# Performance work log

Hardware: AMD Instinct MI355X
Metric: run time of the kernel (lower is better)

The kernel has to match this reference:

```python
import jax, jax.numpy as jnp
import numpy as np

B, T, D_MODEL = 2, 2048, 2048
N_HEAD, N_KV, HD = 32, 8, 64


def _rope_tables(T, hd, base=10000.0):
    # standard rotary tables, (T, hd) with frequencies repeated over both halves
    inv_freq = 1.0 / (base ** (np.arange(0, hd // 2, dtype=np.float32) / (hd // 2)))
    t = np.arange(T, dtype=np.float32)
    freqs = np.outer(t, inv_freq)            # (T, hd/2)
    emb = np.concatenate([freqs, freqs], axis=-1)  # (T, hd)
    return jnp.asarray(np.cos(emb)), jnp.asarray(np.sin(emb))


def setup_inputs() -> dict:
    key = jax.random.key(0)
    ks = jax.random.split(key, 5)
    cos, sin = _rope_tables(T, HD)
    s = 0.02
    return {
        "x": jax.random.normal(ks[0], (B, T, D_MODEL), jnp.float32),
        "cos": cos,
        "sin": sin,
        "Wq": jax.random.normal(ks[1], (N_HEAD * HD, D_MODEL), jnp.float32) * s,
        "Wk": jax.random.normal(ks[2], (N_KV * HD, D_MODEL), jnp.float32) * s,
        "Wv": jax.random.normal(ks[3], (N_KV * HD, D_MODEL), jnp.float32) * s,
        "Wo": jax.random.normal(ks[4], (D_MODEL, N_HEAD * HD), jnp.float32) * s,
    }


def _apply_rope(x, cos, sin):
    # x: (B, H, T, D); cos/sin: (T, D)
    D = x.shape[-1]
    x1, x2 = x[..., : D // 2], x[..., D // 2 :]
    rot = jnp.concatenate([-x2, x1], axis=-1)
    c = cos[: x.shape[-2]][None, None]
    s = sin[: x.shape[-2]][None, None]
    return x * c + rot * s


def reference(x, cos, sin, Wq, Wk, Wv, Wo):
    Bv, Tv, _ = x.shape
    q = (x @ Wq.T).reshape(Bv, Tv, N_HEAD, HD).transpose(0, 2, 1, 3)  # (B,H,T,D)
    k = (x @ Wk.T).reshape(Bv, Tv, N_KV, HD).transpose(0, 2, 1, 3)    # (B,Hkv,T,D)
    v = (x @ Wv.T).reshape(Bv, Tv, N_KV, HD).transpose(0, 2, 1, 3)
    q = _apply_rope(q, cos, sin)
    k = _apply_rope(k, cos, sin)
    repeat = N_HEAD // N_KV
    if repeat > 1:
        k = jnp.repeat(k, repeat, axis=1)
        v = jnp.repeat(v, repeat, axis=1)
    scale = 1.0 / jnp.sqrt(jnp.float32(HD)).astype(x.dtype)
    scores = jnp.einsum("bhqd,bhkd->bhqk", q, k) * scale
    causal = jnp.tril(jnp.ones((Tv, Tv), dtype=bool))
    scores = jnp.where(causal[None, None], scores, jnp.finfo(scores.dtype).min)
    attn = jax.nn.softmax(scores, axis=-1)
    out = jnp.einsum("bhqk,bhkd->bhqd", attn, v)
    out = out.transpose(0, 2, 1, 3).reshape(Bv, Tv, N_HEAD * HD)
    return out @ Wo.T
```

## Files before the change

### kernel.cpp

```cpp
#include <hip/hip_runtime.h>
#include <stdint.h>

#define B_SZ 2
#define T_SEQ 2048
#define DM 2048
#define NH 32
#define NKV 8
#define HD 64
#define QKV_W 3072

typedef unsigned short u16;
typedef __bf16 bf16x8 __attribute__((ext_vector_type(8)));
typedef float floatx4 __attribute__((ext_vector_type(4)));

__device__ __forceinline__ float bf2f(u16 u) {
  union { unsigned u; float f; } v; v.u = ((unsigned)u) << 16; return v.f;
}
__device__ __forceinline__ u16 f2bf(float f) {
  union { float f; unsigned u; } v; v.f = f;
  unsigned r = v.u + 0x7fff + ((v.u >> 16) & 1);
  return (u16)(r >> 16);
}
__device__ __forceinline__ unsigned pk2bf(float hi, float lo) {
  return __builtin_amdgcn_perm(__float_as_uint(hi), __float_as_uint(lo), 0x07060302u);
}
__device__ __forceinline__ float fexp2(float x) {
#if __has_builtin(__builtin_amdgcn_exp2f)
  return __builtin_amdgcn_exp2f(x);
#else
  return exp2f(x);
#endif
}
__device__ __forceinline__ float frcp(float x) {
#if __has_builtin(__builtin_amdgcn_rcpf)
  return __builtin_amdgcn_rcpf(x);
#else
  return 1.0f / x;
#endif
}

__device__ __forceinline__ void gld_lds16(const void* g, void* l) {
  __builtin_amdgcn_global_load_lds(
      (const __attribute__((address_space(1))) unsigned int*)g,
      (__attribute__((address_space(3))) unsigned int*)l, 16, 0, 0);
}

__global__ __launch_bounds__(256) void conv4_kernel(
    const float* __restrict__ x, const float* __restrict__ wq,
    const float* __restrict__ wk, const float* __restrict__ wv,
    u16* __restrict__ xb, u16* __restrict__ wqkvb)
{
  const int N4 = 2097152 + 1048576 + 262144 + 262144;
  ushort4* xb4 = (ushort4*)xb;
  ushort4* wq4 = (ushort4*)wqkvb;
  ushort4* wk4 = (ushort4*)(wqkvb + 2048 * 2048);
  ushort4* wv4 = (ushort4*)(wqkvb + 2560 * 2048);
  int i = blockIdx.x * 256 + threadIdx.x;
  int stride = gridDim.x * 256;
  for (; i < N4; i += stride) {
    const float4* sp; ushort4* dp; int off;
    if (i < 2097152)      { sp = (const float4*)x;  dp = xb4; off = i; }
    else if (i < 3145728) { sp = (const float4*)wq; dp = wq4; off = i - 2097152; }
    else if (i < 3407872) { sp = (const float4*)wk; dp = wk4; off = i - 3145728; }
    else                  { sp = (const float4*)wv; dp = wv4; off = i - 3407872; }
    float4 v = sp[off];
    ushort4 o;
    o.x = f2bf(v.x); o.y = f2bf(v.y); o.z = f2bf(v.z); o.w = f2bf(v.w);
    dp[off] = o;
  }
}

__global__ __launch_bounds__(256) void conv_kernel(
    const float* __restrict__ src, u16* __restrict__ dst, int n4)
{
  int i = blockIdx.x * 256 + threadIdx.x;
  int stride = gridDim.x * 256;
  for (; i < n4; i += stride) {
    float4 v = ((const float4*)src)[i];
    ushort4 o;
    o.x = f2bf(v.x); o.y = f2bf(v.y); o.z = f2bf(v.z); o.w = f2bf(v.w);
    ((ushort4*)dst)[i] = o;
  }
}

__global__ __launch_bounds__(256) void gemm_qkv_kernel(
    const u16* __restrict__ A, const u16* __restrict__ Bt,
    u16* __restrict__ C)
{
  __shared__ __align__(16) u16 sA[128 * 32];
  __shared__ __align__(16) u16 sB[128 * 32];

  const int n0 = blockIdx.x * 128;
  const int m0 = blockIdx.y * 128;
  const int K = 2048;

  const int tid  = threadIdx.x;
  const int lane = tid & 63;
  const int w    = tid >> 6;
  const int wm = w >> 1, wn = w & 1;
  const int lm = lane & 15, lq = lane >> 4;

  floatx4 acc[4][4];
  #pragma unroll
  for (int i = 0; i < 4; i++)
    #pragma unroll
    for (int j = 0; j < 4; j++) { floatx4 z = {0.f,0.f,0.f,0.f}; acc[i][j] = z; }

  const int ar = tid >> 2;
  const int ac = (tid & 3) * 8;
  const u16* Ap0 = A  + (size_t)(m0 + ar) * K + ac;
  const u16* Ap1 = A  + (size_t)(m0 + 64 + ar) * K + ac;
  const u16* Bp0 = Bt + (size_t)(n0 + ar) * K + ac;
  const u16* Bp1 = Bt + (size_t)(n0 + 64 + ar) * K + ac;
  u16* sAd = sA + tid * 8;
  u16* sBd = sB + tid * 8;

  for (int k0 = 0; k0 < K; k0 += 32) {
    gld_lds16(Ap0 + k0, sAd);
    gld_lds16(Ap1 + k0, sAd + 2048);
    gld_lds16(Bp0 + k0, sBd);
    gld_lds16(Bp1 + k0, sBd + 2048);
    __syncthreads();

    bf16x8 af[4], bfr[4];
    #pragma unroll
    for (int mi = 0; mi < 4; mi++)
      af[mi] = *(const bf16x8*)(sA + (wm*64 + mi*16 + lm)*32 + lq*8);
    #pragma unroll
    for (int ni = 0; ni < 4; ni++)
      bfr[ni] = *(const bf16x8*)(sB + (wn*64 + ni*16 + lm)*32 + lq*8);

    #pragma unroll
    for (int mi = 0; mi < 4; mi++)
      #pragma unroll
      for (int ni = 0; ni < 4; ni++)
        acc[mi][ni] = __builtin_amdgcn_mfma_f32_16x16x32_bf16(
            af[mi], bfr[ni], acc[mi][ni], 0, 0, 0);
    __syncthreads();
  }

  #pragma unroll
  for (int mi = 0; mi < 4; mi++)
    #pragma unroll
    for (int ni = 0; ni < 4; ni++)
      #pragma unroll
      for (int r = 0; r < 4; r++) {
        int row = m0 + wm*64 + mi*16 + lq*4 + r;
        int col = n0 + wn*64 + ni*16 + lm;
        C[(size_t)row * QKV_W + col] = f2bf(acc[mi][ni][r]);
      }
}

__global__ __launch_bounds__(256) void gemm_out_kernel(
    const u16* __restrict__ A, const u16* __restrict__ Bt,
    float* __restrict__ C)
{
  __shared__ __align__(16) u16 sA[128 * 32];
  __shared__ __align__(16) u16 sB[128 * 32];

  const int n0 = blockIdx.x * 128;
  const int m0 = blockIdx.y * 128;
  const int K = 2048;

  const int tid  = threadIdx.x;
  const int lane = tid & 63;
  const int w    = tid >> 6;
  const int wm = w >> 1, wn = w & 1;
  const int lm = lane & 15, lq = lane >> 4;

  floatx4 acc[4][4];
  #pragma unroll
  for (int i = 0; i < 4; i++)
    #pragma unroll
    for (int j = 0; j < 4; j++) { floatx4 z = {0.f,0.f,0.f,0.f}; acc[i][j] = z; }

  const int ar = tid >> 2;
  const int ac = (tid & 3) * 8;
  const u16* Ap0 = A  + (size_t)(m0 + ar) * K + ac;
  const u16* Ap1 = A  + (size_t)(m0 + 64 + ar) * K + ac;
  const u16* Bp0 = Bt + (size_t)(n0 + ar) * K + ac;
  const u16* Bp1 = Bt + (size_t)(n0 + 64 + ar) * K + ac;
  u16* sAd = sA + tid * 8;
  u16* sBd = sB + tid * 8;

  for (int k0 = 0; k0 < K; k0 += 32) {
    gld_lds16(Ap0 + k0, sAd);
    gld_lds16(Ap1 + k0, sAd + 2048);
    gld_lds16(Bp0 + k0, sBd);
    gld_lds16(Bp1 + k0, sBd + 2048);
    __syncthreads();

    bf16x8 af[4], bfr[4];
    #pragma unroll
    for (int mi = 0; mi < 4; mi++)
      af[mi] = *(const bf16x8*)(sA + (wm*64 + mi*16 + lm)*32 + lq*8);
    #pragma unroll
    for (int ni = 0; ni < 4; ni++)
      bfr[ni] = *(const bf16x8*)(sB + (wn*64 + ni*16 + lm)*32 + lq*8);

    #pragma unroll
    for (int mi = 0; mi < 4; mi++)
      #pragma unroll
      for (int ni = 0; ni < 4; ni++)
        acc[mi][ni] = __builtin_amdgcn_mfma_f32_16x16x32_bf16(
            af[mi], bfr[ni], acc[mi][ni], 0, 0, 0);
    __syncthreads();
  }

  #pragma unroll
  for (int mi = 0; mi < 4; mi++)
    #pragma unroll
    for (int ni = 0; ni < 4; ni++)
      #pragma unroll
      for (int r = 0; r < 4; r++) {
        int row = m0 + wm*64 + mi*16 + lq*4 + r;
        int col = n0 + wn*64 + ni*16 + lm;
        C[(size_t)row * DM + col] = acc[mi][ni][r];
      }
}

#define QSCALE 0.180336880f
__global__ __launch_bounds__(256) void rope_kernel(
    const u16* __restrict__ qkv, const float* __restrict__ cosf,
    const float* __restrict__ sinf, u16* __restrict__ qb, u16* __restrict__ kb)
{
  const int bt = blockIdx.x;
  const int b = bt / T_SEQ, t = bt % T_SEQ;
  const int tid = threadIdx.x;
  const u16* row = qkv + (size_t)bt * QKV_W;

  #pragma unroll
  for (int i = 0; i < 4; i++) {
    int idx = i * 256 + tid;
    int h = idx >> 5, dp = idx & 31;
    float x1 = bf2f(row[h * 64 + dp]);
    float x2 = bf2f(row[h * 64 + dp + 32]);
    float c = cosf[t * 64 + dp];
    float s = sinf[t * 64 + dp];
    float o1 = (x1 * c - x2 * s) * QSCALE;
    float o2 = (x2 * c + x1 * s) * QSCALE;
    size_t base = ((size_t)(b * NH + h) * T_SEQ + t) * HD + dp;
    qb[base]      = f2bf(o1);
    qb[base + 32] = f2bf(o2);
  }
  {
    int idx = tid;
    int kvh = idx >> 5, dp = idx & 31;
    float x1 = bf2f(row[2048 + kvh * 64 + dp]);
    float x2 = bf2f(row[2048 + kvh * 64 + dp + 32]);
    float c = cosf[t * 64 + dp];
    float s = sinf[t * 64 + dp];
    size_t base = ((size_t)(b * NKV + kvh) * T_SEQ + t) * HD + dp;
    kb[base]      = f2bf(x1 * c - x2 * s);
    kb[base + 32] = f2bf(x2 * c + x1 * s);
  }
}

__global__ __launch_bounds__(256) void vtrans_kernel(
    const u16* __restrict__ qkv, u16* __restrict__ vbt)
{
  __shared__ u16 tile[64][66];
  const int t0  = blockIdx.x * 64;
  const int kvh = blockIdx.y;
  const int b   = blockIdx.z;
  const int tid = threadIdx.x;

  #pragma unroll
  for (int i = 0; i < 16; i++) {
    int idx = i * 256 + tid;
    int r = idx >> 6, c = idx & 63;
    tile[r][c] = qkv[(size_t)(b * T_SEQ + t0 + r) * QKV_W + 2560 + kvh * 64 + c];
  }
  __syncthreads();
  #pragma unroll
  for (int i = 0; i < 16; i++) {
    int idx = i * 256 + tid;
    int d = idx >> 6, c = idx & 63;
    vbt[((size_t)(b * NKV + kvh) * HD + d) * T_SEQ + t0 + c] = tile[c][d];
  }
}

__global__ __launch_bounds__(256, 3) void attn_kernel(
    const u16* __restrict__ qb, const u16* __restrict__ kb,
    const u16* __restrict__ vbt, u16* __restrict__ attn)
{
  __shared__ __align__(16) u16 sK[2][64 * 64];
  __shared__ __align__(16) u16 sV[2][64 * 64];
  __shared__ __align__(16) u16 sP[4][2][16][72];

  const int tid  = threadIdx.x;
  const int lane = tid & 63;
  const int w    = tid >> 6;

  const int l   = blockIdx.x;
  const int b   = l >> 9;
  const int m_  = l & 511;
  const int kv  = m_ & 7;
  const int j   = m_ >> 3;
  const int qt2 = (j & 1) ? (63 - (j >> 1)) : (j >> 1);
  const int h   = kv * 4 + w;
  const int nkt = (qt2 >> 1) + 1;

  const int lm = lane & 15, lq = lane >> 4;
  const int sw = lm & 7;

  bf16x8 qf[2][2];
  {
    const u16* qhead = qb + ((size_t)(b * NH + h) * T_SEQ + qt2 * 32) * HD;
    #pragma unroll
    for (int nq = 0; nq < 2; nq++) {
      const u16* qrow = qhead + (size_t)(nq * 16 + lm) * HD + lq * 8;
      qf[nq][0] = *(const bf16x8*)(qrow);
      qf[nq][1] = *(const bf16x8*)(qrow + 32);
    }
  }

  floatx4 o_acc[2][4];
  #pragma unroll
  for (int i = 0; i < 2; i++)
    #pragma unroll
    for (int jj = 0; jj < 4; jj++) { floatx4 z = {0.f,0.f,0.f,0.f}; o_acc[i][jj] = z; }
  float m_run[2] = {-1e30f, -1e30f};
  float l_run[2] = {0.f, 0.f};

  const u16* kbase = kb  + (size_t)(b * NKV + kv) * T_SEQ * HD;
  const u16* vbt_  = vbt + (size_t)(b * NKV + kv) * HD * T_SEQ;

  const int p0row = tid >> 3,                 p1row = 32 + (tid >> 3);
  const int p0ck  = (tid & 7) ^ (p0row & 7),  p1ck  = (tid & 7) ^ (p1row & 7);
  const u16* kp0 = kbase + (size_t)p0row * HD + p0ck * 8;
  const u16* kp1 = kbase + (size_t)p1row * HD + p1ck * 8;
  const u16* vp0 = vbt_ + (size_t)p0row * T_SEQ + p0ck * 8;
  const u16* vp1 = vbt_ + (size_t)p1row * T_SEQ + p1ck * 8;
  const int d0 = tid * 16, d1 = (256 + tid) * 16;

  gld_lds16(kp0, (char*)sK[0] + d0);
  gld_lds16(kp1, (char*)sK[0] + d1);
  gld_lds16(vp0, (char*)sV[0] + d0);
  gld_lds16(vp1, (char*)sV[0] + d1);

  for (int kt = 0; kt < nkt; kt++) {
    __syncthreads();
    const int cur = kt & 1;
    if (kt + 1 < nkt) {
      const size_t ko = (size_t)(kt + 1) * 64 * HD;
      const int    vo = (kt + 1) * 64;
      gld_lds16(kp0 + ko, (char*)sK[1 - cur] + d0);
      gld_lds16(kp1 + ko, (char*)sK[1 - cur] + d1);
      gld_lds16(vp0 + vo, (char*)sV[1 - cur] + d0);
      gld_lds16(vp1 + vo, (char*)sV[1 - cur] + d1);
    }
    const u16* K = sK[cur];
    const u16* V = sV[cur];
    const bool last = (kt == nkt - 1);

    bf16x8 kf[4][2];
    #pragma unroll
    for (int nt = 0; nt < 4; nt++) {
      kf[nt][0] = *(const bf16x8*)(K + (((nt*16 + lm) * 8 + (lq ^ sw)) << 3));
      kf[nt][1] = *(const bf16x8*)(K + (((nt*16 + lm) * 8 + ((4 + lq) ^ sw)) << 3));
    }

    #pragma unroll
    for (int nq = 0; nq < 2; nq++) {
      floatx4 s_acc[4];
      #pragma unroll
      for (int nt = 0; nt < 4; nt++) {
        floatx4 z = {0.f,0.f,0.f,0.f};
        z = __builtin_amdgcn_mfma_f32_16x16x32_bf16(kf[nt][0], qf[nq][0], z, 0, 0, 0);
        z = __builtin_amdgcn_mfma_f32_16x16x32_bf16(kf[nt][1], qf[nq][1], z, 0, 0, 0);
        s_acc[nt] = z;
      }

      if (last) {
        #pragma unroll
        for (int nt = 0; nt < 4; nt++)
          #pragma unroll
          for (int r = 0; r < 4; r++)
            if (kt * 64 + nt * 16 + lq * 4 + r > qt2 * 32 + nq * 16 + lm)
              s_acc[nt][r] = -1e30f;
      }

      float m01 = fmaxf(fmaxf(s_acc[0][0], s_acc[0][1]), fmaxf(s_acc[0][2], s_acc[0][3]));
      float m23 = fmaxf(fmaxf(s_acc[1][0], s_acc[1][1]), fmaxf(s_acc[1][2], s_acc[1][3]));
      float m45 = fmaxf(fmaxf(s_acc[2][0], s_acc[2][1]), fmaxf(s_acc[2][2], s_acc[2][3]));
      float m67 = fmaxf(fmaxf(s_acc[3][0], s_acc[3][1]), fmaxf(s_acc[3][2], s_acc[3][3]));
      float mloc = fmaxf(fmaxf(m01, m23), fmaxf(m45, m67));
      mloc = fmaxf(mloc, __shfl_xor(mloc, 16));
      mloc = fmaxf(mloc, __shfl_xor(mloc, 32));
      float mnew = fmaxf(m_run[nq], mloc);
      float al = fexp2(m_run[nq] - mnew);

      float rs = 0.f;
      uint2 pk[4];
      #pragma unroll
      for (int nt = 0; nt < 4; nt++) {
        float p0 = fexp2(s_acc[nt][0] - mnew);
        float p1 = fexp2(s_acc[nt][1] - mnew);
        float p2 = fexp2(s_acc[nt][2] - mnew);
        float p3 = fexp2(s_acc[nt][3] - mnew);
        rs += (p0 + p1) + (p2 + p3);
        pk[nt].x = pk2bf(p1, p0);
        pk[nt].y = pk2bf(p3, p2);
      }
      rs += __shfl_xor(rs, 16);
      rs += __shfl_xor(rs, 32);
      l_run[nq] = l_run[nq] * al + rs;
      m_run[nq] = mnew;

      #pragma unroll
      for (int nt = 0; nt < 4; nt++)
        *(uint2*)&sP[w][nq][lm][nt * 16 + lq * 4] = pk[nt];

      #pragma unroll
      for (int r = 0; r < 4; r++) {
        float ar_ = __shfl(al, 4 * lq + r);
        #pragma unroll
        for (int nd = 0; nd < 4; nd++)
          o_acc[nq][nd][r] *= ar_;
      }
    }

    bf16x8 vf[4][2];
    #pragma unroll
    for (int nd = 0; nd < 4; nd++) {
      vf[nd][0] = *(const bf16x8*)(V + (((nd*16 + lm) * 8 + (lq ^ sw)) << 3));
      vf[nd][1] = *(const bf16x8*)(V + (((nd*16 + lm) * 8 + ((4 + lq) ^ sw)) << 3));
    }
    #pragma unroll
    for (int nq = 0; nq < 2; nq++)
      #pragma unroll
      for (int st = 0; st < 2; st++) {
        bf16x8 pf = *(const bf16x8*)(&sP[w][nq][lm][st * 32 + lq * 8]);
        #pragma unroll
        for (int nd = 0; nd < 4; nd++)
          o_acc[nq][nd] = __builtin_amdgcn_mfma_f32_16x16x32_bf16(
              pf, vf[nd][st], o_acc[nq][nd], 0, 0, 0);
      }
  }

  #pragma unroll
  for (int nq = 0; nq < 2; nq++) {
    #pragma unroll
    for (int r = 0; r < 4; r++) {
      float lr = __shfl(l_run[nq], 4 * lq + r);
      float ri = frcp(lr);
      size_t row = (size_t)b * T_SEQ + qt2 * 32 + nq * 16 + lq * 4 + r;
      #pragma unroll
      for (int nd = 0; nd < 4; nd++)
        attn[row * DM + h * HD + nd * 16 + lm] = f2bf(o_acc[nq][nd][r] * ri);
    }
  }
}

extern "C" void kernel_launch(void* const* d_in, const int* in_sizes, int n_in,
                              void* d_out, int out_size, void* d_ws, size_t ws_size,
                              hipStream_t stream)
{
  const float* x    = (const float*)d_in[0];
  const float* cosf = (const float*)d_in[1];
  const float* sinf = (const float*)d_in[2];
  const float* Wq   = (const float*)d_in[3];
  const float* Wk   = (const float*)d_in[4];
  const float* Wv   = (const float*)d_in[5];
  const float* Wo   = (const float*)d_in[6];
  float* out = (float*)d_out;

  char* ws = (char*)d_ws;
  u16* qkvb  = (u16*)(ws + 0);
  u16* attnb = (u16*)(ws + 0);
  u16* qb    = (u16*)(ws + 25165824);
  u16* kb    = (u16*)(ws + 41943040);
  u16* vbt   = (u16*)(ws + 46137344);
  u16* xb    = (u16*)(ws + 50331648);
  u16* wob   = (u16*)(ws + 50331648);
  u16* wqkvb = (u16*)(ws + 67108864);

  dim3 blk(256);
  conv4_kernel<<<dim3(2048), blk, 0, stream>>>(x, Wq, Wk, Wv, xb, wqkvb);

  gemm_qkv_kernel<<<dim3(24, 32), blk, 0, stream>>>(xb, wqkvb, qkvb);

  conv_kernel<<<dim3(1024), blk, 0, stream>>>(Wo, wob, 4194304 / 4);

  rope_kernel<<<dim3(B_SZ * T_SEQ), blk, 0, stream>>>(qkvb, cosf, sinf, qb, kb);
  vtrans_kernel<<<dim3(T_SEQ / 64, NKV, B_SZ), blk, 0, stream>>>(qkvb, vbt);
  attn_kernel<<<dim3(1024), blk, 0, stream>>>(qb, kb, vbt, attnb);
  gemm_out_kernel<<<dim3(16, 32), blk, 0, stream>>>(attnb, wob, out);
}
```

Before: 342.4 us.

## Enlarge attention query tile to 64 rows and feed P from registers via 16x16x16 MFMA

The attention kernel now gives each wave 64 query rows instead of 32, which halves the grid and reuses each loaded K/V tile for twice as many queries. When the 16x16x16 bf16 MFMA builtin exists, the softmax probabilities stay in registers and feed the PV MFMA directly with a transposed output layout, removing the LDS round-trip for P and the per-row alpha shuffles. Causal masking and the block schedule are simplified to 64-row aligned tiles. The trade-offs are more registers per wave (larger accumulators and Q fragments), smaller MFMA instructions, and fewer blocks, which may hurt occupancy and load balance.

After: 412.9 us. +20.6%, slower.

```diff
diff --git a/kernel.cpp b/kernel.cpp
--- a/kernel.cpp
+++ b/kernel.cpp
@@ -11,7 +11,14 @@
 
 typedef unsigned short u16;
 typedef __bf16 bf16x8 __attribute__((ext_vector_type(8)));
+typedef short s16x4 __attribute__((ext_vector_type(4)));
 typedef float floatx4 __attribute__((ext_vector_type(4)));
+
+#if __has_builtin(__builtin_amdgcn_mfma_f32_16x16x16bf16_1k)
+#define HAS_MFMA16 1
+#else
+#define HAS_MFMA16 0
+#endif
 
 __device__ __forceinline__ float bf2f(u16 u) {
   union { unsigned u; float f; } v; v.u = ((unsigned)u) << 16; return v.f;
@@ -23,6 +30,9 @@
 }
 __device__ __forceinline__ unsigned pk2bf(float hi, float lo) {
   return __builtin_amdgcn_perm(__float_as_uint(hi), __float_as_uint(lo), 0x07060302u);
+}
+__device__ __forceinline__ unsigned pk2bf_rne(float hi, float lo) {
+  return ((unsigned)f2bf(hi) << 16) | f2bf(lo);
 }
 __device__ __forceinline__ float fexp2(float x) {
 #if __has_builtin(__builtin_amdgcn_exp2f)
@@ -286,42 +296,44 @@
 {
   __shared__ __align__(16) u16 sK[2][64 * 64];
   __shared__ __align__(16) u16 sV[2][64 * 64];
-  __shared__ __align__(16) u16 sP[4][2][16][72];
+#if !HAS_MFMA16
+  __shared__ __align__(16) u16 sP[4][16][72];
+#endif
 
   const int tid  = threadIdx.x;
   const int lane = tid & 63;
   const int w    = tid >> 6;
 
   const int l   = blockIdx.x;
-  const int b   = l >> 9;
-  const int m_  = l & 511;
-  const int kv  = m_ & 7;
-  const int j   = m_ >> 3;
-  const int qt2 = (j & 1) ? (63 - (j >> 1)) : (j >> 1);
+  const int idx = l & 255;
+  const int b   = idx & 1;
+  const int kv  = (idx >> 1) & 7;
+  const int jj  = idx >> 4;
+  const int qt  = (l < 256) ? jj : (31 - jj);
   const int h   = kv * 4 + w;
-  const int nkt = (qt2 >> 1) + 1;
+  const int nkt = qt + 1;
 
   const int lm = lane & 15, lq = lane >> 4;
   const int sw = lm & 7;
 
-  bf16x8 qf[2][2];
+  bf16x8 qf[4][2];
   {
-    const u16* qhead = qb + ((size_t)(b * NH + h) * T_SEQ + qt2 * 32) * HD;
-    #pragma unroll
-    for (int nq = 0; nq < 2; nq++) {
+    const u16* qhead = qb + ((size_t)(b * NH + h) * T_SEQ + qt * 64) * HD;
+    #pragma unroll
+    for (int nq = 0; nq < 4; nq++) {
       const u16* qrow = qhead + (size_t)(nq * 16 + lm) * HD + lq * 8;
       qf[nq][0] = *(const bf16x8*)(qrow);
       qf[nq][1] = *(const bf16x8*)(qrow + 32);
     }
   }
 
-  floatx4 o_acc[2][4];
-  #pragma unroll
-  for (int i = 0; i < 2; i++)
-    #pragma unroll
-    for (int jj = 0; jj < 4; jj++) { floatx4 z = {0.f,0.f,0.f,0.f}; o_acc[i][jj] = z; }
-  float m_run[2] = {-1e30f, -1e30f};
-  float l_run[2] = {0.f, 0.f};
+  floatx4 o_acc[4][4];
+  #pragma unroll
+  for (int i = 0; i < 4; i++)
+    #pragma unroll
+    for (int j = 0; j < 4; j++) { floatx4 z = {0.f,0.f,0.f,0.f}; o_acc[i][j] = z; }
+  float m_run[4] = {-1e30f, -1e30f, -1e30f, -1e30f};
+  float l_run[4] = {0.f, 0.f, 0.f, 0.f};
 
   const u16* kbase = kb  + (size_t)(b * NKV + kv) * T_SEQ * HD;
   const u16* vbt_  = vbt + (size_t)(b * NKV + kv) * HD * T_SEQ;
@@ -361,8 +373,27 @@
       kf[nt][1] = *(const bf16x8*)(K + (((nt*16 + lm) * 8 + ((4 + lq) ^ sw)) << 3));
     }
 
-    #pragma unroll
-    for (int nq = 0; nq < 2; nq++) {
+#if HAS_MFMA16
+    s16x4 vfrag[4][4];
+    #pragma unroll
+    for (int nt = 0; nt < 4; nt++) {
+      const int ch = (2 * nt + (lq >> 1)) ^ sw;
+      #pragma unroll
+      for (int nd = 0; nd < 4; nd++)
+        vfrag[nt][nd] = *(const s16x4*)((const char*)V +
+            ((((nd * 16 + lm) * 8 + ch) << 4) + ((lq & 1) << 3)));
+    }
+#else
+    bf16x8 vf[4][2];
+    #pragma unroll
+    for (int nd = 0; nd < 4; nd++) {
+      vf[nd][0] = *(const bf16x8*)(V + (((nd*16 + lm) * 8 + (lq ^ sw)) << 3));
+      vf[nd][1] = *(const bf16x8*)(V + (((nd*16 + lm) * 8 + ((4 + lq) ^ sw)) << 3));
+    }
+#endif
+
+    #pragma unroll
+    for (int nq = 0; nq < 4; nq++) {
       floatx4 s_acc[4];
       #pragma unroll
       for (int nt = 0; nt < 4; nt++) {
@@ -377,8 +408,7 @@
         for (int nt = 0; nt < 4; nt++)
           #pragma unroll
           for (int r = 0; r < 4; r++)
-            if (kt * 64 + nt * 16 + lq * 4 + r > qt2 * 32 + nq * 16 + lm)
-              s_acc[nt][r] = -1e30f;
+            if (nt * 16 + lq * 4 + r > nq * 16 + lm) s_acc[nt][r] = -1e30f;
       }
 
       float m01 = fmaxf(fmaxf(s_acc[0][0], s_acc[0][1]), fmaxf(s_acc[0][2], s_acc[0][3]));
@@ -408,10 +438,22 @@
       l_run[nq] = l_run[nq] * al + rs;
       m_run[nq] = mnew;
 
-      #pragma unroll
-      for (int nt = 0; nt < 4; nt++)
-        *(uint2*)&sP[w][nq][lm][nt * 16 + lq * 4] = pk[nt];
-
+#if HAS_MFMA16
+      #pragma unroll
+      for (int nd = 0; nd < 4; nd++)
+        #pragma unroll
+        for (int r = 0; r < 4; r++)
+          o_acc[nq][nd][r] *= al;
+
+      #pragma unroll
+      for (int nt = 0; nt < 4; nt++) {
+        union { uint2 u; s16x4 s; } pu; pu.u = pk[nt];
+        #pragma unroll
+        for (int nd = 0; nd < 4; nd++)
+          o_acc[nq][nd] = __builtin_amdgcn_mfma_f32_16x16x16bf16_1k(
+              vfrag[nt][nd], pu.s, o_acc[nq][nd], 0, 0, 0);
+      }
+#else
       #pragma unroll
       for (int r = 0; r < 4; r++) {
         float ar_ = __shfl(al, 4 * lq + r);
@@ -419,38 +461,48 @@
         for (int nd = 0; nd < 4; nd++)
           o_acc[nq][nd][r] *= ar_;
       }
-    }
-
-    bf16x8 vf[4][2];
-    #pragma unroll
-    for (int nd = 0; nd < 4; nd++) {
-      vf[nd][0] = *(const bf16x8*)(V + (((nd*16 + lm) * 8 + (lq ^ sw)) << 3));
-      vf[nd][1] = *(const bf16x8*)(V + (((nd*16 + lm) * 8 + ((4 + lq) ^ sw)) << 3));
-    }
-    #pragma unroll
-    for (int nq = 0; nq < 2; nq++)
+      #pragma unroll
+      for (int nt = 0; nt < 4; nt++)
+        *(uint2*)&sP[w][lm][nt * 16 + lq * 4] = pk[nt];
       #pragma unroll
       for (int st = 0; st < 2; st++) {
-        bf16x8 pf = *(const bf16x8*)(&sP[w][nq][lm][st * 32 + lq * 8]);
+        bf16x8 pf = *(const bf16x8*)(&sP[w][lm][st * 32 + lq * 8]);
         #pragma unroll
         for (int nd = 0; nd < 4; nd++)
           o_acc[nq][nd] = __builtin_amdgcn_mfma_f32_16x16x32_bf16(
               pf, vf[nd][st], o_acc[nq][nd], 0, 0, 0);
       }
-  }
-
-  #pragma unroll
-  for (int nq = 0; nq < 2; nq++) {
+#endif
+    }
+  }
+
+#if HAS_MFMA16
+  #pragma unroll
+  for (int nq = 0; nq < 4; nq++) {
+    float ri = frcp(l_run[nq]);
+    size_t row = (size_t)b * T_SEQ + qt * 64 + nq * 16 + lm;
+    #pragma unroll
+    for (int nd = 0; nd < 4; nd++) {
+      uint2 o;
+      o.x = pk2bf_rne(o_acc[nq][nd][1] * ri, o_acc[nq][nd][0] * ri);
+      o.y = pk2bf_rne(o_acc[nq][nd][3] * ri, o_acc[nq][nd][2] * ri);
+      *(uint2*)&attn[row * DM + h * HD + nd * 16 + lq * 4] = o;
+    }
+  }
+#else
+  #pragma unroll
+  for (int nq = 0; nq < 4; nq++) {
     #pragma unroll
     for (int r = 0; r < 4; r++) {
       float lr = __shfl(l_run[nq], 4 * lq + r);
       float ri = frcp(lr);
-      size_t row = (size_t)b * T_SEQ + qt2 * 32 + nq * 16 + lq * 4 + r;
+      size_t row = (size_t)b * T_SEQ + qt * 64 + nq * 16 + lq * 4 + r;
       #pragma unroll
       for (int nd = 0; nd < 4; nd++)
         attn[row * DM + h * HD + nd * 16 + lm] = f2bf(o_acc[nq][nd][r] * ri);
     }
   }
+#endif
 }
 
 extern "C" void kernel_launch(void* const* d_in, const int* in_sizes, int n_in,
@@ -485,6 +537,6 @@
 
   rope_kernel<<<dim3(B_SZ * T_SEQ), blk, 0, stream>>>(qkvb, cosf, sinf, qb, kb);
   vtrans_kernel<<<dim3(T_SEQ / 64, NKV, B_SZ), blk, 0, stream>>>(qkvb, vbt);
-  attn_kernel<<<dim3(1024), blk, 0, stream>>>(qb, kb, vbt, attnb);
+  attn_kernel<<<dim3(512), blk, 0, stream>>>(qb, kb, vbt, attnb);
   gemm_out_kernel<<<dim3(16, 32), blk, 0, stream>>>(attnb, wob, out);
 }
```
